# Kernel optimization log

Measured on AMD Instinct MI355X. Metric: run time of the kernel, lower is better.

The kernel has to match this reference:

```python
import jax, jax.numpy as jnp
import numpy as np

B, S, HID = 2, 2048, 4096
H, KVH, D = 32, 8, 128
MAXPOS = 4096


def _rotate_half(x):
    x1, x2 = jnp.split(x, 2, axis=-1)
    return jnp.concatenate([-x2, x1], axis=-1)


def setup_inputs() -> dict:
    key = jax.random.key(0)
    k0, k1, k2, k3, k4 = jax.random.split(key, 5)
    s = 0.02
    hidden_states = jax.random.normal(k0, (B, S, HID), jnp.float32)
    Wq = jax.random.normal(k1, (HID, H * D), jnp.float32) * s
    Wk = jax.random.normal(k2, (HID, KVH * D), jnp.float32) * s
    Wv = jax.random.normal(k3, (HID, KVH * D), jnp.float32) * s
    Wo = jax.random.normal(k4, (H * D, HID), jnp.float32) * s
    past_key_value = jnp.zeros((B, 2, KVH, MAXPOS, D), jnp.float32)
    # RoPE tables (fp32, as asserted in the torch module)
    inv_freq = 1.0 / (10000.0 ** (np.arange(0, D, 2, dtype=np.float64) / D))
    freqs = np.outer(np.arange(S, dtype=np.float64), inv_freq)  # [S, D/2]
    emb = np.concatenate([freqs, freqs], axis=-1)                # [S, D]
    cos = jnp.asarray(np.cos(emb), jnp.float32)
    sin = jnp.asarray(np.sin(emb), jnp.float32)
    return {"hidden_states": hidden_states, "past_key_value": past_key_value,
            "cos": cos, "sin": sin, "Wq": Wq, "Wk": Wk, "Wv": Wv, "Wo": Wo}


def reference(hidden_states, past_key_value, cos, sin, Wq, Wk, Wv, Wo):
    b, s, _ = hidden_states.shape
    # QKV projections (no bias, as in Llama-style attention)
    q = (hidden_states @ Wq).reshape(b, s, H, D)
    k = (hidden_states @ Wk).reshape(b, s, KVH, D)
    v = (hidden_states @ Wv).reshape(b, s, KVH, D)
    # Fused RoPE (qk_norm is identity for standard models)
    c = cos[None, :, None, :]
    sn = sin[None, :, None, :]
    q = q * c + _rotate_half(q) * sn
    k = k * c + _rotate_half(k) * sn
    # KV-cache update (prefill: context_lengths=0, kvcache_start_index=0)
    k_bhsd = k.transpose(0, 2, 1, 3)  # [b, kvh, s, d]
    v_bhsd = v.transpose(0, 2, 1, 3)
    present = past_key_value.at[:, 0, :, :s, :].set(k_bhsd)
    present = present.at[:, 1, :, :s, :].set(v_bhsd)
    # GQA: repeat kv heads to match query heads
    rep = H // KVH
    kr = jnp.repeat(k, rep, axis=2)  # [b, s, H, d]
    vr = jnp.repeat(v, rep, axis=2)
    scores = jnp.einsum("bqhd,bkhd->bhqk", q, kr) / np.float32(np.sqrt(D))
    causal = jnp.tril(jnp.ones((s, s), bool))  # [q, k]
    scores = jnp.where(causal[None, None], scores, jnp.finfo(scores.dtype).min)
    w = jax.nn.softmax(scores.astype(jnp.float32), axis=-1).astype(q.dtype)
    attn = jnp.einsum("bhqk,bkhd->bqhd", w, vr).reshape(b, s, H * D)
    out = attn @ Wo
    return out, present
```

## Files before the change

kernel.cpp:

```cpp
#include <hip/hip_runtime.h>
#include <hip/hip_bf16.h>

typedef unsigned short u16;
typedef __bf16 bf16x8 __attribute__((ext_vector_type(8)));
typedef float  f32x4  __attribute__((ext_vector_type(4)));

__device__ __forceinline__ u16 f2bf(float f) {
    return __builtin_bit_cast(u16, (__bf16)f);
}
__device__ __forceinline__ float b2f(u16 u) {
    return __builtin_bit_cast(float, (unsigned)u << 16);
}
__device__ __forceinline__ f32x4 mfma16(bf16x8 a, bf16x8 b, f32x4 c) {
    return __builtin_amdgcn_mfma_f32_16x16x32_bf16(a, b, c, 0, 0, 0);
}
__device__ __forceinline__ void gl_lds16(const void* g, void* l) {
    __builtin_amdgcn_global_load_lds((const __attribute__((address_space(1))) void*)g,
                                     (__attribute__((address_space(3))) void*)l, 16, 0, 0);
}

__global__ void k_pre(const float* __restrict__ hidden, u16* __restrict__ hiddenB,
                      const float4* __restrict__ past, float4* __restrict__ present4) {
    int bx = blockIdx.x;
    if (bx < 16384) {
        long i = ((long)bx * 256 + threadIdx.x) * 4;
        float4 v = *(const float4*)(hidden + i);
        ushort4 o;
        o.x = f2bf(v.x); o.y = f2bf(v.y); o.z = f2bf(v.z); o.w = f2bf(v.w);
        *(ushort4*)(hiddenB + i) = o;
    } else {
        long i = (long)(bx - 16384) * 256 + threadIdx.x;
        long g = i >> 16;
        long inner = i & 65535;
        long off = g * 131072 + 65536 + inner;
        present4[off] = past[off];
    }
}

__global__ void k_transpose_all(const float* __restrict__ Wq, const float* __restrict__ Wk,
                                const float* __restrict__ Wv, const float* __restrict__ Wo,
                                u16* __restrict__ WqkvT, u16* __restrict__ WoT) {
    __shared__ float t[32][33];
    const int bx = blockIdx.x, k0 = blockIdx.y * 32;
    const float* src; u16* dst; int N; int col;
    if (bx < 128)      { src = Wq; N = 4096; col = bx * 32;         dst = WqkvT; }
    else if (bx < 160) { src = Wk; N = 1024; col = (bx - 128) * 32; dst = WqkvT + 4096L * 4096; }
    else if (bx < 192) { src = Wv; N = 1024; col = (bx - 160) * 32; dst = WqkvT + 5120L * 4096; }
    else               { src = Wo; N = 4096; col = (bx - 192) * 32; dst = WoT; }
    const int tx = threadIdx.x, ty = threadIdx.y;
    #pragma unroll
    for (int i = 0; i < 32; i += 8)
        t[ty + i][tx] = src[(long)(k0 + ty + i) * N + col + tx];
    __syncthreads();
    #pragma unroll
    for (int i = 0; i < 32; i += 8)
        dst[(long)(col + ty + i) * 4096 + k0 + tx] = f2bf(t[tx][ty + i]);
}

template<int BNF, int OBF16>
__global__ void __launch_bounds__(512, 2)
k_gemm8(const u16* __restrict__ A, const u16* __restrict__ Bt,
        void* __restrict__ Cv, int M, int N, int K, int gx)
{
    extern __shared__ u16 lds[];
    const int nwg = gridDim.x;
    const int bid = blockIdx.x;
    const int swzb = (bid & 7) * (nwg >> 3) + (bid >> 3);
    const long m0 = (long)(swzb / gx) * 256;
    const long n0 = (long)(swzb % gx) * (64 * BNF);

    const int t = threadIdx.x;
    const int l = t & 63;
    const int w = t >> 6;
    const int wm = w >> 2, wn = w & 3;

    const int srow = t >> 3;
    const int scol = ((t & 7) ^ (srow & 7)) << 3;
    const u16* ap = A  + (m0 + srow) * (long)K + scol;
    const u16* bp = Bt + (n0 + srow) * (long)K + scol;
    const int sL = t * 8;

    const int swz0 = (((l >> 4) ^ (l & 7)) << 3);
    const int swz1 = ((((l >> 4) | 4) ^ (l & 7)) << 3);
    const int arow = wm * 128 + (l & 15);
    const int aoff0 = arow * 64 + swz0, aoff1 = arow * 64 + swz1;
    const int brow = wn * (16 * BNF) + (l & 15);
    const int boff0 = brow * 64 + swz0, boff1 = brow * 64 + swz1;

    f32x4 acc[8][BNF];
    #pragma unroll
    for (int i = 0; i < 8; ++i)
        #pragma unroll
        for (int j = 0; j < BNF; ++j) acc[i][j] = (f32x4){0.f, 0.f, 0.f, 0.f};

    const int nt = K >> 6;
    #pragma unroll
    for (int k = 0; k < 4; ++k)
        gl_lds16(ap + (long)k * 64 * K, &lds[sL + 4096 * k]);
    #pragma unroll
    for (int k = 0; k < BNF; ++k)
        gl_lds16(bp + (long)k * 64 * K, &lds[32768 + sL + 4096 * k]);

    for (int kt = 0; kt < nt; ++kt) {
        const int d = kt & 1;
        const int dA = d * 16384, dB = 32768 + d * 4096 * BNF;
        if (kt + 1 < nt) {
            const int e = d ^ 1;
            const u16* a1 = ap + (kt + 1) * 64;
            const u16* b1 = bp + (kt + 1) * 64;
            #pragma unroll
            for (int k = 0; k < 4; ++k)
                gl_lds16(a1 + (long)k * 64 * K, &lds[e * 16384 + sL + 4096 * k]);
            #pragma unroll
            for (int k = 0; k < BNF; ++k)
                gl_lds16(b1 + (long)k * 64 * K, &lds[32768 + e * 4096 * BNF + sL + 4096 * k]);
            if constexpr (BNF == 3) asm volatile("s_waitcnt vmcnt(7)" ::: "memory");
            else                    asm volatile("s_waitcnt vmcnt(8)" ::: "memory");
        } else {
            asm volatile("s_waitcnt vmcnt(0)" ::: "memory");
        }
        __builtin_amdgcn_sched_barrier(0);
        __builtin_amdgcn_s_barrier();
        __builtin_amdgcn_sched_barrier(0);

        bf16x8 bfr[BNF][2];
        #pragma unroll
        for (int nf = 0; nf < BNF; ++nf) {
            bfr[nf][0] = *(const bf16x8*)&lds[dB + boff0 + nf * 1024];
            bfr[nf][1] = *(const bf16x8*)&lds[dB + boff1 + nf * 1024];
        }
        {
            bf16x8 af[2][2];
            #pragma unroll
            for (int mm = 0; mm < 2; ++mm) {
                af[mm][0] = *(const bf16x8*)&lds[dA + aoff0 + mm * 1024];
                af[mm][1] = *(const bf16x8*)&lds[dA + aoff1 + mm * 1024];
            }
            asm volatile("s_waitcnt lgkmcnt(0)" ::: "memory");
            __builtin_amdgcn_sched_barrier(0);
            __builtin_amdgcn_s_setprio(1);
            #pragma unroll
            for (int mm = 0; mm < 2; ++mm)
                #pragma unroll
                for (int nf = 0; nf < BNF; ++nf) {
                    acc[mm][nf] = mfma16(af[mm][0], bfr[nf][0], acc[mm][nf]);
                    acc[mm][nf] = mfma16(af[mm][1], bfr[nf][1], acc[mm][nf]);
                }
            __builtin_amdgcn_s_setprio(0);
            __builtin_amdgcn_sched_barrier(0);
        }
        #pragma unroll
        for (int q = 1; q < 4; ++q) {
            bf16x8 af[2][2];
            #pragma unroll
            for (int mm = 0; mm < 2; ++mm) {
                af[mm][0] = *(const bf16x8*)&lds[dA + aoff0 + (q * 2 + mm) * 1024];
                af[mm][1] = *(const bf16x8*)&lds[dA + aoff1 + (q * 2 + mm) * 1024];
            }
            __builtin_amdgcn_sched_barrier(0);
            __builtin_amdgcn_s_barrier();
            asm volatile("s_waitcnt lgkmcnt(0)" ::: "memory");
            __builtin_amdgcn_sched_barrier(0);
            __builtin_amdgcn_s_setprio(1);
            #pragma unroll
            for (int mm = 0; mm < 2; ++mm)
                #pragma unroll
                for (int nf = 0; nf < BNF; ++nf) {
                    acc[q * 2 + mm][nf] = mfma16(af[mm][0], bfr[nf][0], acc[q * 2 + mm][nf]);
                    acc[q * 2 + mm][nf] = mfma16(af[mm][1], bfr[nf][1], acc[q * 2 + mm][nf]);
                }
            __builtin_amdgcn_s_setprio(0);
            __builtin_amdgcn_sched_barrier(0);
        }
        __builtin_amdgcn_s_barrier();
        __builtin_amdgcn_sched_barrier(0);
    }

    #pragma unroll
    for (int mf = 0; mf < 8; ++mf)
        #pragma unroll
        for (int nf = 0; nf < BNF; ++nf) {
            long row = m0 + wm * 128 + mf * 16 + ((l >> 4) << 2);
            long cb = row * N + n0 + wn * (16 * BNF) + nf * 16 + (l & 15);
            if constexpr (OBF16) {
                u16* cp = (u16*)Cv + cb;
                #pragma unroll
                for (int r = 0; r < 4; ++r) cp[(long)r * N] = f2bf(acc[mf][nf][r]);
            } else {
                float* cp = (float*)Cv + cb;
                #pragma unroll
                for (int r = 0; r < 4; ++r) cp[(long)r * N] = acc[mf][nf][r];
            }
        }
}

__global__ void k_rope_scatter(const u16* __restrict__ qkv, const float* __restrict__ cosb,
                               const float* __restrict__ sinb, u16* __restrict__ Qb,
                               u16* __restrict__ Kb, u16* __restrict__ Vt,
                               float* __restrict__ present)
{
    long idx = (long)blockIdx.x * 256 + threadIdx.x;
    int pg   = (int)(idx & 15);
    int rem  = (int)(idx >> 4);
    int slot = rem % 48;
    int tok  = rem / 48;
    int b = tok >> 11, s = tok & 2047;
    int pair = pg * 4;

    const u16* base = qkv + (long)tok * 6144 + slot * 128 + pair;
    ushort4 xu1 = *(const ushort4*)(base);
    ushort4 xu2 = *(const ushort4*)(base + 64);
    float4 x1 = {b2f(xu1.x), b2f(xu1.y), b2f(xu1.z), b2f(xu1.w)};
    float4 x2 = {b2f(xu2.x), b2f(xu2.y), b2f(xu2.z), b2f(xu2.w)};

    if (slot < 40) {
        float4 c  = *(const float4*)(cosb + s * 128 + pair);
        float4 sn = *(const float4*)(sinb + s * 128 + pair);
        float4 y1, y2;
        y1.x = x1.x * c.x - x2.x * sn.x;  y2.x = x2.x * c.x + x1.x * sn.x;
        y1.y = x1.y * c.y - x2.y * sn.y;  y2.y = x2.y * c.y + x1.y * sn.y;
        y1.z = x1.z * c.z - x2.z * sn.z;  y2.z = x2.z * c.z + x1.z * sn.z;
        y1.w = x1.w * c.w - x2.w * sn.w;  y2.w = x2.w * c.w + x1.w * sn.w;
        if (slot < 32) {
            const float sc = 0.0883883476483184f;
            long qoff = (((long)b * 32 + slot) * 2048 + s) * 128 + pair;
            ushort4 o1, o2;
            o1.x = f2bf(y1.x * sc); o1.y = f2bf(y1.y * sc);
            o1.z = f2bf(y1.z * sc); o1.w = f2bf(y1.w * sc);
            o2.x = f2bf(y2.x * sc); o2.y = f2bf(y2.y * sc);
            o2.z = f2bf(y2.z * sc); o2.w = f2bf(y2.w * sc);
            *(ushort4*)(Qb + qoff)      = o1;
            *(ushort4*)(Qb + qoff + 64) = o2;
        } else {
            int kvh = slot - 32;
            long koff = (((long)b * 8 + kvh) * 2048 + s) * 128 + pair;
            ushort4 o1, o2;
            o1.x = f2bf(y1.x); o1.y = f2bf(y1.y); o1.z = f2bf(y1.z); o1.w = f2bf(y1.w);
            o2.x = f2bf(y2.x); o2.y = f2bf(y2.y); o2.z = f2bf(y2.z); o2.w = f2bf(y2.w);
            *(ushort4*)(Kb + koff)      = o1;
            *(ushort4*)(Kb + koff + 64) = o2;
            long poff = ((((long)b * 2 + 0) * 8 + kvh) * 4096 + s) * 128 + pair;
            *(float4*)(present + poff)      = y1;
            *(float4*)(present + poff + 64) = y2;
        }
    } else {
        int kvh = slot - 40;
        long poff = ((((long)b * 2 + 1) * 8 + kvh) * 4096 + s) * 128 + pair;
        *(float4*)(present + poff)      = x1;
        *(float4*)(present + poff + 64) = x2;
        long voff = (((long)b * 8 + kvh) * 128 + pair) * 2048 + s;
        Vt[voff]             = xu1.x;
        Vt[voff + 1 * 2048]  = xu1.y;
        Vt[voff + 2 * 2048]  = xu1.z;
        Vt[voff + 3 * 2048]  = xu1.w;
        Vt[voff + 64 * 2048] = xu2.x;
        Vt[voff + 65 * 2048] = xu2.y;
        Vt[voff + 66 * 2048] = xu2.z;
        Vt[voff + 67 * 2048] = xu2.w;
    }
}

__global__ void __launch_bounds__(256, 2)
k_attn(const u16* __restrict__ Qb, const u16* __restrict__ Kb,
       const u16* __restrict__ Vt, u16* __restrict__ attnB)
{
    __shared__ __align__(16) u16 Ks[64 * 128];
    __shared__ __align__(16) u16 Vs[128 * 64];
    const int l = threadIdx.x & 63;
    const int w = threadIdx.x >> 6;
    const int h = blockIdx.y, b = blockIdx.z;
    const int p = blockIdx.x;
    const int kvh = h >> 2;
    u16* Psw = &Ks[w * 2048];

    const long kbase = ((long)b * 8 + kvh) * (2048L * 128);
    const long vbase = ((long)b * 8 + kvh) * (128L * 2048);
    f32x4 zero = {0.f, 0.f, 0.f, 0.f};

    for (int half = 0; half < 2; ++half) {
        const int qt = half ? (15 - p) : p;
        const int q0 = qt * 128;

        const long qbase = (((long)b * 32 + h) * 2048 + q0 + w * 32) * 128;
        bf16x8 qf[2][4];
        #pragma unroll
        for (int mi = 0; mi < 2; ++mi)
            #pragma unroll
            for (int kk = 0; kk < 4; ++kk)
                qf[mi][kk] = *(const bf16x8*)(Qb + qbase + (long)(mi * 16 + (l & 15)) * 128
                                              + kk * 32 + ((l >> 4) << 3));

        f32x4 o[2][8];
        float mst[2][4], lst[2][4];
        #pragma unroll
        for (int mi = 0; mi < 2; ++mi) {
            #pragma unroll
            for (int j = 0; j < 8; ++j) o[mi][j] = zero;
            #pragma unroll
            for (int r = 0; r < 4; ++r) { mst[mi][r] = -3.0e38f; lst[mi][r] = 0.f; }
        }

        const int nkt = (q0 >> 6) + 2;
        for (int kt = 0; kt < nkt; ++kt) {
            const int k0 = kt * 64;
            __syncthreads();
            #pragma unroll
            for (int i = 0; i < 4; ++i) {
                int c = w * 4 + i;
                int row = c * 4 + (l >> 4);
                int lg = ((l & 15) ^ (row & 15)) << 3;
                gl_lds16(Kb + kbase + (long)(k0 + row) * 128 + lg, &Ks[c * 512]);
            }
            #pragma unroll
            for (int i = 0; i < 4; ++i) {
                int c = w * 4 + i;
                int row = c * 8 + (l >> 3);
                int lg = ((l & 7) ^ (row & 7)) << 3;
                gl_lds16(Vt + vbase + (long)row * 2048 + k0 + lg, &Vs[c * 512]);
            }
            __syncthreads();

            f32x4 s[2][4];
            #pragma unroll
            for (int mi = 0; mi < 2; ++mi)
                #pragma unroll
                for (int nf = 0; nf < 4; ++nf) s[mi][nf] = zero;
            #pragma unroll
            for (int kk = 0; kk < 4; ++kk) {
                bf16x8 kf[4];
                #pragma unroll
                for (int nf = 0; nf < 4; ++nf) {
                    int row = nf * 16 + (l & 15);
                    int ph = (kk * 4 + (l >> 4)) ^ (row & 15);
                    kf[nf] = *(const bf16x8*)&Ks[row * 128 + ph * 8];
                }
                __builtin_amdgcn_s_setprio(1);
                #pragma unroll
                for (int mi = 0; mi < 2; ++mi)
                    #pragma unroll
                    for (int nf = 0; nf < 4; ++nf)
                        s[mi][nf] = mfma16(qf[mi][kk], kf[nf], s[mi][nf]);
                __builtin_amdgcn_s_setprio(0);
            }
            #pragma unroll
            for (int mi = 0; mi < 2; ++mi)
                #pragma unroll
                for (int nf = 0; nf < 4; ++nf)
                    #pragma unroll
                    for (int r = 0; r < 4; ++r) {
                        int rowg = q0 + w * 32 + mi * 16 + ((l >> 4) << 2) + r;
                        int colg = k0 + nf * 16 + (l & 15);
                        if (colg > rowg) s[mi][nf][r] = -1.0e30f;
                    }
            #pragma unroll
            for (int mi = 0; mi < 2; ++mi)
                #pragma unroll
                for (int r = 0; r < 4; ++r) {
                    float t = fmaxf(fmaxf(s[mi][0][r], s[mi][1][r]),
                                    fmaxf(s[mi][2][r], s[mi][3][r]));
                    t = fmaxf(t, __shfl_xor(t, 1));
                    t = fmaxf(t, __shfl_xor(t, 2));
                    t = fmaxf(t, __shfl_xor(t, 4));
                    t = fmaxf(t, __shfl_xor(t, 8));
                    float nm = fmaxf(mst[mi][r], t);
                    float sc = __expf(mst[mi][r] - nm);
                    mst[mi][r] = nm;
                    lst[mi][r] *= sc;
                    #pragma unroll
                    for (int nf2 = 0; nf2 < 8; ++nf2) o[mi][nf2][r] *= sc;
                }
            __syncthreads();
            #pragma unroll
            for (int mi = 0; mi < 2; ++mi)
                #pragma unroll
                for (int nf = 0; nf < 4; ++nf)
                    #pragma unroll
                    for (int r = 0; r < 4; ++r) {
                        float pv = __expf(s[mi][nf][r] - mst[mi][r]);
                        lst[mi][r] += pv;
                        int row = mi * 16 + ((l >> 4) << 2) + r;
                        int col = nf * 16 + (l & 15);
                        Psw[row * 64 + (((col >> 3) ^ (row & 7)) << 3) + (col & 7)] = f2bf(pv);
                    }
            #pragma unroll
            for (int kk2 = 0; kk2 < 2; ++kk2) {
                bf16x8 pa[2];
                #pragma unroll
                for (int mi = 0; mi < 2; ++mi) {
                    int row = mi * 16 + (l & 15);
                    int ph = (kk2 * 4 + (l >> 4)) ^ (row & 7);
                    pa[mi] = *(const bf16x8*)&Psw[row * 64 + ph * 8];
                }
                #pragma unroll
                for (int nf2 = 0; nf2 < 8; ++nf2) {
                    int vrow = nf2 * 16 + (l & 15);
                    int ph = (kk2 * 4 + (l >> 4)) ^ (vrow & 7);
                    bf16x8 vf = *(const bf16x8*)&Vs[vrow * 64 + ph * 8];
                    __builtin_amdgcn_s_setprio(1);
                    #pragma unroll
                    for (int mi = 0; mi < 2; ++mi)
                        o[mi][nf2] = mfma16(pa[mi], vf, o[mi][nf2]);
                    __builtin_amdgcn_s_setprio(0);
                }
            }
        }

        #pragma unroll
        for (int mi = 0; mi < 2; ++mi)
            #pragma unroll
            for (int r = 0; r < 4; ++r) {
                float t = lst[mi][r];
                t += __shfl_xor(t, 1);
                t += __shfl_xor(t, 2);
                t += __shfl_xor(t, 4);
                t += __shfl_xor(t, 8);
                lst[mi][r] = 1.0f / t;
            }
        #pragma unroll
        for (int mi = 0; mi < 2; ++mi)
            #pragma unroll
            for (int nf2 = 0; nf2 < 8; ++nf2)
                #pragma unroll
                for (int r = 0; r < 4; ++r) {
                    long row = (long)b * 2048 + q0 + w * 32 + mi * 16 + ((l >> 4) << 2) + r;
                    attnB[row * 4096 + h * 128 + nf2 * 16 + (l & 15)] =
                        f2bf(o[mi][nf2][r] * lst[mi][r]);
                }
    }
}

extern "C" void kernel_launch(void* const* d_in, const int* in_sizes, int n_in,
                              void* d_out, int out_size, void* d_ws, size_t ws_size,
                              hipStream_t stream)
{
    (void)in_sizes; (void)n_in; (void)out_size; (void)ws_size;
    const float* hidden = (const float*)d_in[0];
    const float* past   = (const float*)d_in[1];
    const float* cosb   = (const float*)d_in[2];
    const float* sinb   = (const float*)d_in[3];
    const float* Wq     = (const float*)d_in[4];
    const float* Wk     = (const float*)d_in[5];
    const float* Wv     = (const float*)d_in[6];
    const float* Wo     = (const float*)d_in[7];
    float* out     = (float*)d_out;
    float* present = out + 16777216L;

    char* ws = (char*)d_ws;
    u16*  hiddenB = (u16*)(ws);
    u16*  WqkvT   = (u16*)(ws + 33554432L);
    u16*  WoT     = (u16*)(ws + 83886080L);
    u16*  QKVb    = (u16*)(ws + 117440512L);
    u16*  Kb      = (u16*)(ws + 218103808L);
    u16*  Vt      = (u16*)(ws + 226492416L);
    u16*  Qbuf    = hiddenB;
    u16*  attnB   = QKVb;

    static bool attr_done = false;
    if (!attr_done) {
        hipFuncSetAttribute((const void*)k_gemm8<3, 1>,
                            hipFuncAttributeMaxDynamicSharedMemorySize, 114688);
        hipFuncSetAttribute((const void*)k_gemm8<4, 0>,
                            hipFuncAttributeMaxDynamicSharedMemorySize, 131072);
        attr_done = true;
    }

    k_pre<<<24576, 256, 0, stream>>>(hidden, hiddenB, (const float4*)past, (float4*)present);
    k_transpose_all<<<dim3(320, 128), dim3(32, 8), 0, stream>>>(Wq, Wk, Wv, Wo, WqkvT, WoT);
    k_gemm8<3, 1><<<512, 512, 114688, stream>>>(hiddenB, WqkvT, (void*)QKVb,
                                                4096, 6144, 4096, 32);
    k_rope_scatter<<<12288, 256, 0, stream>>>(QKVb, cosb, sinb, Qbuf, Kb, Vt, present);
    k_attn<<<dim3(8, 32, 2), 256, 0, stream>>>(Qbuf, Kb, Vt, attnB);
    k_gemm8<4, 0><<<256, 512, 131072, stream>>>(attnB, WoT, (void*)out,
                                                4096, 4096, 4096, 16);
}
```

Before: 598.7 us.

## Add half-tile pipelined GEMM kernel for output projection

Adds a new 256x256-tile GEMM for the Wo projection. It splits each k-tile into A and B halves and interleaves global-to-LDS loads for upcoming tiles between quarter MFMA blocks, with barriers at each phase. The aim is finer-grained overlap of memory loads with matrix-core work than the older double-buffered loop gives. Each k-tile now needs more barriers, and the existing kernel only gets macro cleanup.

```diff
diff --git a/kernel.cpp b/kernel.cpp
--- a/kernel.cpp
+++ b/kernel.cpp
@@ -57,6 +57,142 @@
         dst[(long)(col + ty + i) * 4096 + k0 + tx] = f2bf(t[tx][ty + i]);
 }
 
+#define ABAR() do { __builtin_amdgcn_sched_barrier(0); __builtin_amdgcn_s_barrier(); \
+                    __builtin_amdgcn_sched_barrier(0); } while (0)
+#define LGKM0() do { asm volatile("s_waitcnt lgkmcnt(0)" ::: "memory"); \
+                     __builtin_amdgcn_sched_barrier(0); } while (0)
+
+__global__ void __launch_bounds__(512, 2)
+k_gemm8ph(const u16* __restrict__ A, const u16* __restrict__ Bt,
+          float* __restrict__ C, int M, int N, int K, int gx)
+{
+    extern __shared__ u16 lds[];
+    const int nwg = gridDim.x;
+    const int bid = blockIdx.x;
+    const int swzb = (bid & 7) * (nwg >> 3) + (bid >> 3);
+    const long m0 = (long)(swzb / gx) * 256;
+    const long n0 = (long)(swzb % gx) * 256;
+
+    const int t = threadIdx.x;
+    const int l = t & 63;
+    const int w = t >> 6;
+    const int wm = w >> 2, wn = w & 3;
+
+    const int srow = t >> 3;
+    const int scol = ((t & 7) ^ (srow & 7)) << 3;
+    const u16* aph[2] = { A  + (m0 + 0   + srow) * (long)K + scol,
+                          A  + (m0 + 128 + srow) * (long)K + scol };
+    const u16* bph[2] = { Bt + (n0 + 0   + srow) * (long)K + scol,
+                          Bt + (n0 + 128 + srow) * (long)K + scol };
+
+    const int swz0 = (((l >> 4) ^ (l & 7)) << 3);
+    const int swz1 = ((((l >> 4) | 4) ^ (l & 7)) << 3);
+    const int arowb = (wm * 64 + (l & 15)) * 64;
+    const int browb = (wn * 32 + (l & 15)) * 64;
+
+    f32x4 acc[8][4];
+    #pragma unroll
+    for (int i = 0; i < 8; ++i)
+        #pragma unroll
+        for (int j = 0; j < 4; ++j) acc[i][j] = (f32x4){0.f, 0.f, 0.f, 0.f};
+
+    bf16x8 a[4][2], b0[2][2], b1[2][2];
+
+    auto stA = [&](int d, int h, int kt) {
+        const u16* s = aph[h] + (long)kt * 64;
+        gl_lds16(s,              &lds[(d * 2 + h) * 8192 + t * 8]);
+        gl_lds16(s + 64L * K,    &lds[(d * 2 + h) * 8192 + 4096 + t * 8]);
+    };
+    auto stB = [&](int d, int h, int kt) {
+        const u16* s = bph[h] + (long)kt * 64;
+        gl_lds16(s,              &lds[32768 + (d * 2 + h) * 8192 + t * 8]);
+        gl_lds16(s + 64L * K,    &lds[32768 + (d * 2 + h) * 8192 + 4096 + t * 8]);
+    };
+    auto rdA = [&](int d, int h) {
+        const int base = (d * 2 + h) * 8192;
+        #pragma unroll
+        for (int mf = 0; mf < 4; ++mf) {
+            a[mf][0] = *(const bf16x8*)&lds[base + arowb + mf * 1024 + swz0];
+            a[mf][1] = *(const bf16x8*)&lds[base + arowb + mf * 1024 + swz1];
+        }
+    };
+    auto rdB = [&](int d, int h, bf16x8 (&bb)[2][2]) {
+        const int base = 32768 + (d * 2 + h) * 8192;
+        #pragma unroll
+        for (int nf = 0; nf < 2; ++nf) {
+            bb[nf][0] = *(const bf16x8*)&lds[base + browb + nf * 1024 + swz0];
+            bb[nf][1] = *(const bf16x8*)&lds[base + browb + nf * 1024 + swz1];
+        }
+    };
+    auto mfmaQ = [&](int qm, int qn, bf16x8 (&bb)[2][2]) {
+        __builtin_amdgcn_s_setprio(1);
+        #pragma unroll
+        for (int mf = 0; mf < 4; ++mf)
+            #pragma unroll
+            for (int nf = 0; nf < 2; ++nf) {
+                acc[qm * 4 + mf][qn * 2 + nf] =
+                    mfma16(a[mf][0], bb[nf][0], acc[qm * 4 + mf][qn * 2 + nf]);
+                acc[qm * 4 + mf][qn * 2 + nf] =
+                    mfma16(a[mf][1], bb[nf][1], acc[qm * 4 + mf][qn * 2 + nf]);
+            }
+        __builtin_amdgcn_s_setprio(0);
+        __builtin_amdgcn_sched_barrier(0);
+    };
+
+    const int nt = K >> 6;
+    stA(0, 0, 0); stB(0, 0, 0); stB(0, 1, 0); stA(0, 1, 0);
+    stA(1, 0, 1); stB(1, 0, 1); stB(1, 1, 1); stA(1, 1, 1);
+    asm volatile("s_waitcnt vmcnt(8)" ::: "memory");
+    __builtin_amdgcn_sched_barrier(0);
+    __builtin_amdgcn_s_barrier();
+    __builtin_amdgcn_sched_barrier(0);
+
+    for (int kt = 0; kt < nt; kt += 2) {
+        const bool g = (kt + 2) < nt;
+        #pragma unroll
+        for (int hh = 0; hh < 2; ++hh) {
+            const int d = hh;
+            const int ktp = kt + 2 + hh;
+            rdA(d, 0); rdB(d, 0, b0);
+            ABAR(); LGKM0();
+            mfmaQ(0, 0, b0);
+            ABAR();
+            rdB(d, 1, b1);
+            if (g) { stA(d, 0, ktp); stB(d, 0, ktp); }
+            ABAR(); LGKM0();
+            mfmaQ(0, 1, b1);
+            ABAR();
+            rdA(d, 1);
+            if (g) stB(d, 1, ktp);
+            ABAR(); LGKM0();
+            mfmaQ(1, 0, b0);
+            ABAR();
+            if (g) {
+                stA(d, 1, ktp);
+                asm volatile("s_waitcnt vmcnt(8)" ::: "memory");
+            } else {
+                asm volatile("s_waitcnt vmcnt(0)" ::: "memory");
+            }
+            ABAR();
+            mfmaQ(1, 1, b1);
+            ABAR();
+        }
+    }
+
+    #pragma unroll
+    for (int i8 = 0; i8 < 8; ++i8) {
+        const int qm = i8 >> 2, mf = i8 & 3;
+        #pragma unroll
+        for (int j4 = 0; j4 < 4; ++j4) {
+            const int qn = j4 >> 1, nf = j4 & 1;
+            long row = m0 + qm * 128 + wm * 64 + mf * 16 + ((l >> 4) << 2);
+            float* cp = C + row * N + n0 + qn * 128 + wn * 32 + nf * 16 + (l & 15);
+            #pragma unroll
+            for (int r = 0; r < 4; ++r) cp[(long)r * N] = acc[i8][j4][r];
+        }
+    }
+}
+
 template<int BNF, int OBF16>
 __global__ void __launch_bounds__(512, 2)
 k_gemm8(const u16* __restrict__ A, const u16* __restrict__ Bt,
@@ -119,9 +255,7 @@
         } else {
             asm volatile("s_waitcnt vmcnt(0)" ::: "memory");
         }
-        __builtin_amdgcn_sched_barrier(0);
-        __builtin_amdgcn_s_barrier();
-        __builtin_amdgcn_sched_barrier(0);
+        ABAR();
 
         bf16x8 bfr[BNF][2];
         #pragma unroll
@@ -136,8 +270,7 @@
                 af[mm][0] = *(const bf16x8*)&lds[dA + aoff0 + mm * 1024];
                 af[mm][1] = *(const bf16x8*)&lds[dA + aoff1 + mm * 1024];
             }
-            asm volatile("s_waitcnt lgkmcnt(0)" ::: "memory");
-            __builtin_amdgcn_sched_barrier(0);
+            LGKM0();
             __builtin_amdgcn_s_setprio(1);
             #pragma unroll
             for (int mm = 0; mm < 2; ++mm)
@@ -157,10 +290,8 @@
                 af[mm][0] = *(const bf16x8*)&lds[dA + aoff0 + (q * 2 + mm) * 1024];
                 af[mm][1] = *(const bf16x8*)&lds[dA + aoff1 + (q * 2 + mm) * 1024];
             }
-            __builtin_amdgcn_sched_barrier(0);
-            __builtin_amdgcn_s_barrier();
-            asm volatile("s_waitcnt lgkmcnt(0)" ::: "memory");
-            __builtin_amdgcn_sched_barrier(0);
+            ABAR();
+            LGKM0();
             __builtin_amdgcn_s_setprio(1);
             #pragma unroll
             for (int mm = 0; mm < 2; ++mm)
@@ -172,8 +303,7 @@
             __builtin_amdgcn_s_setprio(0);
             __builtin_amdgcn_sched_barrier(0);
         }
-        __builtin_amdgcn_s_barrier();
-        __builtin_amdgcn_sched_barrier(0);
+        ABAR();
     }
 
     #pragma unroll
@@ -459,7 +589,7 @@
     if (!attr_done) {
         hipFuncSetAttribute((const void*)k_gemm8<3, 1>,
                             hipFuncAttributeMaxDynamicSharedMemorySize, 114688);
-        hipFuncSetAttribute((const void*)k_gemm8<4, 0>,
+        hipFuncSetAttribute((const void*)k_gemm8ph,
                             hipFuncAttributeMaxDynamicSharedMemorySize, 131072);
         attr_done = true;
     }
@@ -470,6 +600,5 @@
                                                 4096, 6144, 4096, 32);
     k_rope_scatter<<<12288, 256, 0, stream>>>(QKVb, cosb, sinb, Qbuf, Kb, Vt, present);
     k_attn<<<dim3(8, 32, 2), 256, 0, stream>>>(Qbuf, Kb, Vt, attnB);
-    k_gemm8<4, 0><<<256, 512, 131072, stream>>>(attnB, WoT, (void*)out,
-                                                4096, 4096, 4096, 16);
-}
+    k_gemm8ph<<<256, 512, 131072, stream>>>(attnB, WoT, out, 4096, 4096, 4096, 16);
+}
```

Result: faster. 581.1 us (-2.9%).
